# Performance work log

Hardware: AMD Instinct MI355X
Metric: run time of the kernel (lower is better)

## Reference

```python
import jax, jax.numpy as jnp
import numpy as np

B, T, D, H, E, K, OUT = 4, 1024, 512, 1024, 8, 2, 512
TEMP = 1.0      # current_temperature == max_temperature at init
LN_EPS = 1e-5   # torch LayerNorm default
MI_EPS = 1e-6


def _ln(x, g, b):
    mu = jnp.mean(x, -1, keepdims=True)
    var = jnp.mean((x - mu) ** 2, -1, keepdims=True)
    return (x - mu) * jax.lax.rsqrt(var + LN_EPS) * g + b


def setup_inputs() -> dict:
    key = jax.random.key(0)
    ks = jax.random.split(key, 16)
    s = 0.02
    return {
        "x": jax.random.normal(ks[0], (B, T, D), jnp.float32),
        # Router
        "Wmap": jax.random.normal(ks[1], (D, D * E), jnp.float32) * s,
        "bmap": jnp.zeros((D * E,), jnp.float32),
        "Wr": jax.random.normal(ks[2], (D, D), jnp.float32) * s,
        "br": jnp.zeros((D,), jnp.float32),
        # Stacked expert MLP (3 linear+GELU+LayerNorm blocks; dropout is eval no-op)
        "W1": jax.random.normal(ks[3], (E, D, H), jnp.float32) * s,
        "b1": jnp.zeros((E, H), jnp.float32),
        "g1": jnp.ones((E, H), jnp.float32),
        "beta1": jnp.zeros((E, H), jnp.float32),
        "W2": jax.random.normal(ks[4], (E, H, H), jnp.float32) * s,
        "b2": jnp.zeros((E, H), jnp.float32),
        "g2": jnp.ones((E, H), jnp.float32),
        "beta2": jnp.zeros((E, H), jnp.float32),
        "W3": jax.random.normal(ks[5], (E, H, H), jnp.float32) * s,
        "b3": jnp.zeros((E, H), jnp.float32),
        "g3": jnp.ones((E, H), jnp.float32),
        "beta3": jnp.zeros((E, H), jnp.float32),
        # out_linear: Linear(H, OUT) + GELU + LayerNorm(OUT)
        "Wo": jax.random.normal(ks[6], (H, OUT), jnp.float32) * s,
        "bo": jnp.zeros((OUT,), jnp.float32),
        "go": jnp.ones((OUT,), jnp.float32),
        "beta_o": jnp.zeros((OUT,), jnp.float32),
    }


def reference(x, Wmap, bmap, Wr, br,
              W1, b1, g1, beta1, W2, b2, g2, beta2, W3, b3, g3, beta3,
              Wo, bo, go, beta_o):
    Bx, Tx, Dx = x.shape
    Ex = W1.shape[0]
    # Router: per-token, per-expert embeddings [B,T,E,D]
    re = (x @ Wmap + bmap).reshape(Bx, Tx, Ex, Dx) @ Wr + br
    # Laplace gating (faithful to source: topk of NEGATED exp(-d/T))
    dist = jnp.linalg.norm(x[:, :, None, :] - re, axis=-1)   # [B,T,E]
    sim = jnp.exp(-dist / TEMP)
    vals, idx = jax.lax.top_k(-sim, K)                       # vals are negative
    probs = vals / jnp.sum(vals, -1, keepdims=True)          # neg/neg -> positive, sums to 1

    N = Bx * Tx
    xf = x.reshape(N, Dx)
    pf = probs.reshape(N, K)
    idf = idx.reshape(N, K)
    # Dense gate matrix [N,E]: gating weight per token per expert (0 if unselected).
    gate = jnp.zeros((N, Ex), x.dtype).at[jnp.arange(N)[:, None], idf].add(pf)

    # Stacked expert MLP on all tokens; gating zeros out unselected experts (same math
    # as the masked gather/index_add dispatch in the source).
    h = jax.nn.gelu(jnp.einsum('nd,edh->neh', xf, W1) + b1, approximate=False)
    h = _ln(h, g1, beta1)
    h = jax.nn.gelu(jnp.einsum('neh,ehf->nef', h, W2) + b2, approximate=False)
    h = _ln(h, g2, beta2)
    h = jax.nn.gelu(jnp.einsum('neh,ehf->nef', h, W3) + b3, approximate=False)
    h = _ln(h, g3, beta3)                                    # [N,E,H]
    combined = jnp.einsum('ne,neh->nh', gate, h).reshape(Bx, Tx, -1)

    out = _ln(jax.nn.gelu(combined @ Wo + bo, approximate=False), go, beta_o)

    # Stand-in for RunningMarginalMI.compute_mi_loss (source class unavailable):
    # negative mutual information between marginal and per-token slot distributions.
    pm = jnp.mean(pf, 0)
    ent_loss = jnp.sum(pm * jnp.log(pm + MI_EPS)) - jnp.mean(jnp.sum(pf * jnp.log(pf + MI_EPS), -1))
    return out, ent_loss
```

## Files before the change

### kernel.cpp

```cpp
#include <hip/hip_runtime.h>
#include <hip/hip_bf16.h>
#include <math.h>

typedef __hip_bfloat16 bf16;
typedef unsigned short u16;
typedef __attribute__((ext_vector_type(8))) short short8;
typedef __attribute__((ext_vector_type(4))) float f32x4;

#define NTOK 4096
#define DD   512
#define EE   8
#define DE   4096
#define HH   1024
#define OUTD 512
#define ATOT 8192
#define APAD 8320
#define MAXT 72
#define FCAP 1024
#define DMARGIN 1e-4
#define RSPLIT 4

struct Tile { int e, row0, rows; };

__device__ __forceinline__ float b2f(u16 u){ return __uint_as_float(((unsigned)u)<<16); }

__device__ __forceinline__ float gelu_f(float x){
  return 0.5f * x * (1.0f + erff(x * 0.7071067811865476f));
}

__device__ __forceinline__ void gl2lds(const bf16* g, bf16* l){
  __builtin_amdgcn_global_load_lds((const __attribute__((address_space(1))) void*)g,
                                   (__attribute__((address_space(3))) void*)l, 16, 0, 0);
}

__device__ __forceinline__ f32x4 mfma16(short8 a, short8 b, f32x4 c){
  return __builtin_amdgcn_mfma_f32_16x16x32_bf16(a, b, c, 0, 0, 0);
}

template<bool GATHER>
__device__ __forceinline__ void kloop(const bf16* __restrict__ A, int lda,
                                      const int* __restrict__ rowmap, int m0,
                                      const bf16* __restrict__ BT, int ldb, int n0,
                                      int K, bf16* As, bf16* Bs, f32x4 acc[4][4]){
  const int t = threadIdx.x;
  const int r = t>>2;
  const int sw = (t&3) ^ ((t>>3)&3);
  int ar0 = m0 + r, ar1 = m0 + 64 + r;
  if (GATHER){
    ar0 = rowmap[ar0 < ATOT ? ar0 : ATOT-1];
    ar1 = rowmap[ar1 < ATOT ? ar1 : ATOT-1];
  }
  const bf16* ap0 = A + (long)ar0*lda + sw*8;
  const bf16* ap1 = A + (long)ar1*lda + sw*8;
  const bf16* bp0 = BT + (long)(n0 + r)*ldb + sw*8;
  const bf16* bp1 = bp0 + (long)64*ldb;
  const int wave = t>>6, lane = t&63;
  const int qr = wave>>1, qc = wave&1, ln = lane&15, kq = lane>>4;
  const int slot = kq ^ ((ln>>1)&3);
  const bf16* ard = As + (qr*64 + ln)*32 + slot*8;
  const bf16* brd = Bs + (qc*64 + ln)*32 + slot*8;
  gl2lds(ap0, As + t*8);
  gl2lds(ap1, As + 2048 + t*8);
  gl2lds(bp0, Bs + t*8);
  gl2lds(bp1, Bs + 2048 + t*8);
  for (int k0 = 0; k0 < K; k0 += 32){
    __syncthreads();
    short8 a[4], b[4];
    #pragma unroll
    for (int i=0;i<4;i++) a[i] = *(const short8*)(ard + i*512);
    #pragma unroll
    for (int j=0;j<4;j++) b[j] = *(const short8*)(brd + j*512);
    __syncthreads();
    int k1 = k0 + 32;
    if (k1 < K){
      gl2lds(ap0 + k1, As + t*8);
      gl2lds(ap1 + k1, As + 2048 + t*8);
      gl2lds(bp0 + k1, Bs + t*8);
      gl2lds(bp1 + k1, Bs + 2048 + t*8);
    }
    #pragma unroll
    for (int i=0;i<4;i++)
      #pragma unroll
      for (int j=0;j<4;j++)
        acc[i][j] = mfma16(a[i], b[j], acc[i][j]);
  }
}

__device__ __forceinline__ void kloop2(const bf16* __restrict__ A0, const bf16* __restrict__ A1,
                                       int lda, int m0,
                                       const bf16* __restrict__ B0, const bf16* __restrict__ B1,
                                       int ldb, int n0, int K,
                                       bf16* As0, bf16* As1, bf16* Bs0, bf16* Bs1,
                                       f32x4 acc[4][4]){
  const int t = threadIdx.x;
  const int r = t>>2;
  const int sw = (t&3) ^ ((t>>3)&3);
  const long aoff0 = (long)(m0 + r)*lda + sw*8;
  const long aoff1 = (long)(m0 + 64 + r)*lda + sw*8;
  const long boff0 = (long)(n0 + r)*ldb + sw*8;
  const long boff1 = boff0 + (long)64*ldb;
  const int wave = t>>6, lane = t&63;
  const int qr = wave>>1, qc = wave&1, ln = lane&15, kq = lane>>4;
  const int slot = kq ^ ((ln>>1)&3);
  const int ao = (qr*64 + ln)*32 + slot*8;
  const int bo = (qc*64 + ln)*32 + slot*8;
  gl2lds(A0 + aoff0, As0 + t*8);
  gl2lds(A0 + aoff1, As0 + 2048 + t*8);
  gl2lds(A1 + aoff0, As1 + t*8);
  gl2lds(A1 + aoff1, As1 + 2048 + t*8);
  gl2lds(B0 + boff0, Bs0 + t*8);
  gl2lds(B0 + boff1, Bs0 + 2048 + t*8);
  gl2lds(B1 + boff0, Bs1 + t*8);
  gl2lds(B1 + boff1, Bs1 + 2048 + t*8);
  for (int k0 = 0; k0 < K; k0 += 32){
    __syncthreads();
    short8 a0[4], a1[4], b0[4], b1[4];
    #pragma unroll
    for (int i=0;i<4;i++){
      a0[i] = *(const short8*)(As0 + ao + i*512);
      a1[i] = *(const short8*)(As1 + ao + i*512);
    }
    #pragma unroll
    for (int j=0;j<4;j++){
      b0[j] = *(const short8*)(Bs0 + bo + j*512);
      b1[j] = *(const short8*)(Bs1 + bo + j*512);
    }
    __syncthreads();
    int k1 = k0 + 32;
    if (k1 < K){
      gl2lds(A0 + aoff0 + k1, As0 + t*8);
      gl2lds(A0 + aoff1 + k1, As0 + 2048 + t*8);
      gl2lds(A1 + aoff0 + k1, As1 + t*8);
      gl2lds(A1 + aoff1 + k1, As1 + 2048 + t*8);
      gl2lds(B0 + boff0 + k1, Bs0 + t*8);
      gl2lds(B0 + boff1 + k1, Bs0 + 2048 + t*8);
      gl2lds(B1 + boff0 + k1, Bs1 + t*8);
      gl2lds(B1 + boff1 + k1, Bs1 + 2048 + t*8);
    }
    #pragma unroll
    for (int i=0;i<4;i++)
      #pragma unroll
      for (int j=0;j<4;j++){
        acc[i][j] = mfma16(a0[i], b0[j], acc[i][j]);
        acc[i][j] = mfma16(a0[i], b1[j], acc[i][j]);
        acc[i][j] = mfma16(a1[i], b0[j], acc[i][j]);
      }
  }
}

__device__ __forceinline__ void kloop3(const bf16* __restrict__ A0, const bf16* __restrict__ A1,
                                       const bf16* __restrict__ A2, int lda, int m0,
                                       const bf16* __restrict__ B0, const bf16* __restrict__ B1,
                                       const bf16* __restrict__ B2, int ldb, int n0, int K,
                                       bf16* As0, bf16* As1, bf16* As2,
                                       bf16* Bs0, bf16* Bs1, bf16* Bs2,
                                       f32x4 acc[4][4]){
  const int t = threadIdx.x;
  const int r = t>>2;
  const int sw = (t&3) ^ ((t>>3)&3);
  const long aoff0 = (long)(m0 + r)*lda + sw*8;
  const long aoff1 = (long)(m0 + 64 + r)*lda + sw*8;
  const long boff0 = (long)(n0 + r)*ldb + sw*8;
  const long boff1 = boff0 + (long)64*ldb;
  const int wave = t>>6, lane = t&63;
  const int qr = wave>>1, qc = wave&1, ln = lane&15, kq = lane>>4;
  const int slot = kq ^ ((ln>>1)&3);
  const int ao = (qr*64 + ln)*32 + slot*8;
  const int bo = (qc*64 + ln)*32 + slot*8;
  gl2lds(A0 + aoff0, As0 + t*8);
  gl2lds(A0 + aoff1, As0 + 2048 + t*8);
  gl2lds(A1 + aoff0, As1 + t*8);
  gl2lds(A1 + aoff1, As1 + 2048 + t*8);
  gl2lds(A2 + aoff0, As2 + t*8);
  gl2lds(A2 + aoff1, As2 + 2048 + t*8);
  gl2lds(B0 + boff0, Bs0 + t*8);
  gl2lds(B0 + boff1, Bs0 + 2048 + t*8);
  gl2lds(B1 + boff0, Bs1 + t*8);
  gl2lds(B1 + boff1, Bs1 + 2048 + t*8);
  gl2lds(B2 + boff0, Bs2 + t*8);
  gl2lds(B2 + boff1, Bs2 + 2048 + t*8);
  for (int k0 = 0; k0 < K; k0 += 32){
    __syncthreads();
    short8 a0[4], a1[4], a2[4], b0[4], b1[4], b2[4];
    #pragma unroll
    for (int i=0;i<4;i++){
      a0[i] = *(const short8*)(As0 + ao + i*512);
      a1[i] = *(const short8*)(As1 + ao + i*512);
      a2[i] = *(const short8*)(As2 + ao + i*512);
    }
    #pragma unroll
    for (int j=0;j<4;j++){
      b0[j] = *(const short8*)(Bs0 + bo + j*512);
      b1[j] = *(const short8*)(Bs1 + bo + j*512);
      b2[j] = *(const short8*)(Bs2 + bo + j*512);
    }
    __syncthreads();
    int k1 = k0 + 32;
    if (k1 < K){
      gl2lds(A0 + aoff0 + k1, As0 + t*8);
      gl2lds(A0 + aoff1 + k1, As0 + 2048 + t*8);
      gl2lds(A1 + aoff0 + k1, As1 + t*8);
      gl2lds(A1 + aoff1 + k1, As1 + 2048 + t*8);
      gl2lds(A2 + aoff0 + k1, As2 + t*8);
      gl2lds(A2 + aoff1 + k1, As2 + 2048 + t*8);
      gl2lds(B0 + boff0 + k1, Bs0 + t*8);
      gl2lds(B0 + boff1 + k1, Bs0 + 2048 + t*8);
      gl2lds(B1 + boff0 + k1, Bs1 + t*8);
      gl2lds(B1 + boff1 + k1, Bs1 + 2048 + t*8);
      gl2lds(B2 + boff0 + k1, Bs2 + t*8);
      gl2lds(B2 + boff1 + k1, Bs2 + 2048 + t*8);
    }
    #pragma unroll
    for (int i=0;i<4;i++)
      #pragma unroll
      for (int j=0;j<4;j++){
        acc[i][j] = mfma16(a0[i], b0[j], acc[i][j]);
        acc[i][j] = mfma16(a0[i], b1[j], acc[i][j]);
        acc[i][j] = mfma16(a1[i], b0[j], acc[i][j]);
        acc[i][j] = mfma16(a0[i], b2[j], acc[i][j]);
        acc[i][j] = mfma16(a1[i], b1[j], acc[i][j]);
        acc[i][j] = mfma16(a2[i], b0[j], acc[i][j]);
      }
  }
}

#define EPI_SETUP \
  const int t = threadIdx.x, wave=t>>6, lane=t&63; \
  const int qr=wave>>1, qc=wave&1, ln=lane&15, kq=lane>>4; (void)qr;

#define ACC_INIT \
  f32x4 acc[4][4]; \
  _Pragma("unroll") for (int i=0;i<4;i++) _Pragma("unroll") for (int j=0;j<4;j++) \
    acc[i][j] = (f32x4){0.f,0.f,0.f,0.f};

__device__ __forceinline__ void split3_body(const float* __restrict__ in,
    bf16* __restrict__ oh, bf16* __restrict__ om, bf16* __restrict__ ol, int b, int n4){
  int i = b*256 + threadIdx.x;
  if (i >= n4) return;
  float4 v = ((const float4*)in)[i];
  float vv[4] = {v.x, v.y, v.z, v.w};
  u16 hs[4], ms[4], ls[4];
  #pragma unroll
  for (int c=0;c<4;c++){
    bf16 h = __float2bfloat16(vv[c]); float r1 = vv[c] - __bfloat162float(h);
    bf16 m = __float2bfloat16(r1);    float r2 = r1 - __bfloat162float(m);
    bf16 l = __float2bfloat16(r2);
    hs[c]=*(u16*)&h; ms[c]=*(u16*)&m; ls[c]=*(u16*)&l;
  }
  ((ushort4*)oh)[i] = (ushort4){hs[0],hs[1],hs[2],hs[3]};
  ((ushort4*)om)[i] = (ushort4){ms[0],ms[1],ms[2],ms[3]};
  ((ushort4*)ol)[i] = (ushort4){ls[0],ls[1],ls[2],ls[3]};
}

__device__ __forceinline__ void tsplit3_body(const float* __restrict__ in,
    bf16* __restrict__ oh, bf16* __restrict__ om, bf16* __restrict__ ol,
    int R, int C, int bx, int by, float* tile ){
  int r0 = by*64, c0 = bx*64;
  int t = threadIdx.x, lr = t>>4, lc = (t&15)*4;
  #pragma unroll
  for (int it=0; it<4; it++){
    int rr = it*16 + lr;
    float4 v = *(const float4*)(in + (long)(r0+rr)*C + c0 + lc);
    tile[rr*65+lc]=v.x; tile[rr*65+lc+1]=v.y; tile[rr*65+lc+2]=v.z; tile[rr*65+lc+3]=v.w;
  }
  __syncthreads();
  #pragma unroll
  for (int it=0; it<4; it++){
    int cc = it*16 + lr;
    u16 hs[4], ms[4], ls[4];
    #pragma unroll
    for (int j=0;j<4;j++){
      float v = tile[(lc+j)*65+cc];
      bf16 h = __float2bfloat16(v); float r1 = v - __bfloat162float(h);
      bf16 m = __float2bfloat16(r1); float r2 = r1 - __bfloat162float(m);
      bf16 l = __float2bfloat16(r2);
      hs[j]=*(u16*)&h; ms[j]=*(u16*)&m; ls[j]=*(u16*)&l;
    }
    long oi = (long)(c0+cc)*R + r0 + lc;
    *(ushort4*)((u16*)oh + oi) = (ushort4){hs[0],hs[1],hs[2],hs[3]};
    *(ushort4*)((u16*)om + oi) = (ushort4){ms[0],ms[1],ms[2],ms[3]};
    *(ushort4*)((u16*)ol + oi) = (ushort4){ls[0],ls[1],ls[2],ls[3]};
  }
}

__device__ __forceinline__ void cvtT_body(const float* __restrict__ in,
    bf16* __restrict__ out, int R, int C, int bx, int by, int bz, float* tile){
  long zb = (long)bz * R * C;
  int r0 = by*64, c0 = bx*64;
  int t = threadIdx.x, lr = t>>4, lc = (t&15)*4;
  #pragma unroll
  for (int it=0; it<4; it++){
    int rr = it*16 + lr;
    float4 v = *(const float4*)(in + zb + (long)(r0+rr)*C + c0 + lc);
    tile[rr*65+lc]=v.x; tile[rr*65+lc+1]=v.y; tile[rr*65+lc+2]=v.z; tile[rr*65+lc+3]=v.w;
  }
  __syncthreads();
  #pragma unroll
  for (int it=0; it<4; it++){
    int cc = it*16 + lr;
    u16 hs[4];
    #pragma unroll
    for (int j=0;j<4;j++){
      bf16 h = __float2bfloat16(tile[(lc+j)*65+cc]);
      hs[j]=*(u16*)&h;
    }
    *(ushort4*)((u16*)out + zb + (long)(c0+cc)*R + r0 + lc) = (ushort4){hs[0],hs[1],hs[2],hs[3]};
  }
}

__device__ __forceinline__ void cvec_body(const float* __restrict__ bmap,
    const float* __restrict__ Wr, const float* __restrict__ br, float* __restrict__ cvec, int b){
  int id = b*256 + threadIdx.x;
  int e = id >> 9, j = id & 511;
  float s = 0.f;
  for (int k=0;k<512;k++) s += bmap[e*512+k] * Wr[k*512 + j];
  cvec[id] = s + br[j];
}

__global__ __launch_bounds__(256) void k_prep(const float* __restrict__ x,
    const float* __restrict__ Wmap, const float* __restrict__ Wr,
    const float* __restrict__ bmap, const float* __restrict__ br,
    const float* __restrict__ W1, const float* __restrict__ W2,
    const float* __restrict__ W3, const float* __restrict__ Wo,
    bf16* xh, bf16* xm, bf16* xl,
    bf16* Wm_h, bf16* Wm_m, bf16* Wm_l,
    bf16* WrT_h, bf16* WrT_m, bf16* WrT_l, float* cvec,
    bf16* W1T, bf16* W2T, bf16* W3T, bf16* WoT){
  __shared__ float tile[64*65];
  int b = blockIdx.x;
  if (b < 2048){ split3_body(x, xh, xm, xl, b, 524288); return; }
  b -= 2048;
  if (b < 2048){ split3_body(Wmap, Wm_h, Wm_m, Wm_l, b, 524288); return; }
  b -= 2048;
  if (b < 64){ tsplit3_body(Wr, WrT_h, WrT_m, WrT_l, 512, 512, b&7, b>>3, tile); return; }
  b -= 64;
  if (b < 16){ cvec_body(bmap, Wr, br, cvec, b); return; }
  b -= 16;
  if (b < 1024){ cvtT_body(W1, W1T, 512, 1024, b&15, (b>>4)&7, b>>7, tile); return; }
  b -= 1024;
  if (b < 2048){ cvtT_body(W2, W2T, 1024, 1024, b&15, (b>>4)&15, b>>8, tile); return; }
  b -= 2048;
  if (b < 2048){ cvtT_body(W3, W3T, 1024, 1024, b&15, (b>>4)&15, b>>8, tile); return; }
  b -= 2048;
  cvtT_body(Wo, WoT, 1024, 512, b&7, b>>3, 0, tile);
}
#define PREP_BLOCKS 9424

__global__ __launch_bounds__(256) void k_gemm_MT(
    const bf16* __restrict__ Rh, const bf16* __restrict__ Rm, const bf16* __restrict__ Rl,
    const bf16* __restrict__ Wh, const bf16* __restrict__ Wm, const bf16* __restrict__ Wl,
    bf16* __restrict__ MTh, bf16* __restrict__ MTm, float* __restrict__ M32){
  __shared__ __align__(16) bf16 As0[4096], As1[4096], As2[4096],
                                Bs0[4096], Bs1[4096], Bs2[4096];
  int m0 = blockIdx.x*128, n0 = blockIdx.y*128, e = blockIdx.z;
  ACC_INIT
  kloop3(Rh, Rm, Rl, 512, m0, Wh + e*512, Wm + e*512, Wl + e*512, DE, n0, 512,
         As0, As1, As2, Bs0, Bs1, Bs2, acc);
  EPI_SETUP
  int cg[4];
  #pragma unroll
  for (int j=0;j<4;j++) cg[j] = n0 + qc*64 + j*16 + ln;
  long eb = (long)e*512*512;
  #pragma unroll
  for (int i=0;i<4;i++)
    #pragma unroll
    for (int r=0;r<4;r++){
      long base = eb + (long)(m0 + qr*64 + i*16 + kq*4 + r) * 512;
      #pragma unroll
      for (int j=0;j<4;j++){
        float v = acc[i][j][r];
        bf16 h = __float2bfloat16(v); float r1 = v - __bfloat162float(h);
        bf16 m = __float2bfloat16(r1);
        MTh[base + cg[j]] = h; MTm[base + cg[j]] = m; M32[base + cg[j]] = v;
      }
    }
}

__global__ __launch_bounds__(256) void k_gemm_re(
    const bf16* __restrict__ xh, const bf16* __restrict__ xm,
    const bf16* __restrict__ MTh, const bf16* __restrict__ MTm,
    const float* __restrict__ cvec, const float* __restrict__ x, double* __restrict__ dist2){
  __shared__ __align__(16) bf16 As0[4096], As1[4096], Bs0[4096], Bs1[4096];
  int m0 = blockIdx.x*128, n0 = blockIdx.y*128, e = blockIdx.z;
  ACC_INIT
  long eb = (long)e*512*512;
  kloop2(xh, xm, 512, m0, MTh + eb, MTm + eb, 512, n0, 512,
         As0, As1, Bs0, Bs1, acc);
  EPI_SETUP
  int cg[4]; float cv[4];
  #pragma unroll
  for (int j=0;j<4;j++){ cg[j] = n0 + qc*64 + j*16 + ln; cv[j] = cvec[e*512 + cg[j]]; }
  #pragma unroll
  for (int i=0;i<4;i++)
    #pragma unroll
    for (int r=0;r<4;r++){
      int rg = m0 + qr*64 + i*16 + kq*4 + r;
      const float* xr = x + (long)rg*512;
      double s = 0.0;
      #pragma unroll
      for (int j=0;j<4;j++){
        float re = acc[i][j][r] + cv[j];
        float d  = xr[cg[j]] - re;
        s += (double)d * (double)d;
      }
      s += __shfl_xor(s,1); s += __shfl_xor(s,2); s += __shfl_xor(s,4); s += __shfl_xor(s,8);
      if (ln == 0) atomicAdd(&dist2[(long)rg*EE + e], s);
    }
}

__global__ __launch_bounds__(256) void k_gemm_exp(const Tile* __restrict__ table,
    const bf16* __restrict__ A, int lda, const int* __restrict__ rowmap,
    const bf16* __restrict__ Wt, long wstride, int ldb, int K,
    const float* __restrict__ bias, int ncols, bf16* __restrict__ out, int ldo){
  Tile tc = table[blockIdx.x];
  if (tc.e < 0) return;
  __shared__ __align__(16) bf16 As[4096], Bs[4096];
  int n0 = blockIdx.y*128;
  ACC_INIT
  const bf16* BT = Wt + (long)tc.e*wstride;
  if (rowmap) kloop<true >(A, lda, rowmap, tc.row0, BT, ldb, n0, K, As, Bs, acc);
  else        kloop<false>(A, lda, nullptr, tc.row0, BT, ldb, n0, K, As, Bs, acc);
  EPI_SETUP
  const float* bp = bias + (long)tc.e*ncols;
  int cg[4]; float bv[4];
  #pragma unroll
  for (int j=0;j<4;j++){ cg[j] = n0 + qc*64 + j*16 + ln; bv[j] = bp[cg[j]]; }
  #pragma unroll
  for (int i=0;i<4;i++)
    #pragma unroll
    for (int r=0;r<4;r++){
      int rl = qr*64 + i*16 + kq*4 + r;
      if (rl < tc.rows){
        bf16* op = out + (long)(tc.row0 + rl)*ldo;
        #pragma unroll
        for (int j=0;j<4;j++)
          op[cg[j]] = __float2bfloat16(gelu_f(acc[i][j][r] + bv[j]));
      }
    }
}

__global__ __launch_bounds__(256) void k_gemm_go(const bf16* __restrict__ A,
    const bf16* __restrict__ WoT, const float* __restrict__ bias, bf16* __restrict__ out){
  __shared__ __align__(16) bf16 As[4096], Bs[4096];
  int m0 = blockIdx.x*128, n0 = blockIdx.y*128;
  ACC_INIT
  kloop<false>(A, HH, nullptr, m0, WoT, HH, n0, HH, As, Bs, acc);
  EPI_SETUP
  int cg[4]; float bv[4];
  #pragma unroll
  for (int j=0;j<4;j++){ cg[j] = n0 + qc*64 + j*16 + ln; bv[j] = bias[cg[j]]; }
  #pragma unroll
  for (int i=0;i<4;i++)
    #pragma unroll
    for (int r=0;r<4;r++){
      long base = (long)(m0 + qr*64 + i*16 + kq*4 + r) * OUTD;
      #pragma unroll
      for (int j=0;j<4;j++)
        out[base + cg[j]] = __float2bfloat16(gelu_f(acc[i][j][r] + bv[j]));
    }
}

__global__ __launch_bounds__(256) void k_select(const double* __restrict__ dist2,
    float* __restrict__ selp, int* __restrict__ seli, int* __restrict__ counts,
    float* __restrict__ entacc, int* __restrict__ flaglist, int* __restrict__ nflag){
  __shared__ int hc[EE];
  int t = threadIdx.x;
  if (t < EE) hc[t] = 0;
  __syncthreads();
  int n = blockIdx.x*256 + t;
  double d0 = -1.0, d1 = -1.0, d2 = -1.0; int i0 = 0, i1 = 0;
  #pragma unroll
  for (int e=0;e<EE;e++){
    double d = sqrt(dist2[(long)n*EE + e]);
    if (d > d0){ d2 = d1; d1 = d0; i1 = i0; d0 = d; i0 = e; }
    else if (d > d1){ d2 = d1; d1 = d; i1 = e; }
    else if (d > d2){ d2 = d; }
  }
  if (d1 - d2 < DMARGIN){ int p = atomicAdd(nflag, 1); flaglist[p & (FCAP-1)] = n; }
  double s0 = exp(-d0), s1 = exp(-d1);
  double den = s0 + s1;
  float p0 = (float)(s0/den), p1 = (float)(s1/den);
  selp[2*n] = p0; selp[2*n+1] = p1;
  seli[2*n] = i0; seli[2*n+1] = i1;
  atomicAdd(&hc[i0], 1); atomicAdd(&hc[i1], 1);
  float a0 = p0, a1 = p1;
  float a2 = p0*logf(p0+1e-6f) + p1*logf(p1+1e-6f);
  #pragma unroll
  for (int m=32;m;m>>=1){ a0 += __shfl_down(a0,m); a1 += __shfl_down(a1,m); a2 += __shfl_down(a2,m); }
  if ((t&63)==0){ atomicAdd(&entacc[0], a0); atomicAdd(&entacc[1], a1); atomicAdd(&entacc[2], a2); }
  __syncthreads();
  if (t < EE) atomicAdd(&counts[t], hc[t]);
}

__global__ __launch_bounds__(256) void k_rescue(const int* __restrict__ flaglist,
    const int* __restrict__ nflag, const float* __restrict__ x,
    const float* __restrict__ M32, const float* __restrict__ cvec,
    double* __restrict__ rbuf4){
  __shared__ float xs[512];
  __shared__ double wsum[4];
  int t = threadIdx.x, w = t>>6, l = t&63;
  int nf = *nflag; if (nf > FCAP) nf = FCAP;
  int work = nf * EE * RSPLIT;
  for (int wid = blockIdx.x; wid < work; wid += gridDim.x){
    int pid = wid >> 2, chunk = wid & (RSPLIT-1);
    int f = pid >> 3, e = pid & 7;
    int n = flaglist[f];
    xs[t] = x[(long)n*512 + t]; xs[t+256] = x[(long)n*512 + 256 + t];
    __syncthreads();
    const float* Me = M32 + ((long)e << 18);
    const float* xp = xs + l*8;
    float x0=xp[0], x1=xp[1], x2=xp[2], x3=xp[3], x4=xp[4], x5=xp[5], x6=xp[6], x7=xp[7];
    double s = 0.0;
    int j0 = chunk*128 + w*32;
    for (int rb = 0; rb < 32; rb += 8){
      double d[8];
      #pragma unroll
      for (int rr=0; rr<8; rr++){
        const float* Mr = Me + (long)(j0 + rb + rr)*512 + l*8;
        float4 a = *(const float4*)Mr, b = *(const float4*)(Mr+4);
        d[rr] = (double)a.x*x0 + (double)a.y*x1 + (double)a.z*x2 + (double)a.w*x3
              + (double)b.x*x4 + (double)b.y*x5 + (double)b.z*x6 + (double)b.w*x7;
      }
      #pragma unroll
      for (int m=32;m;m>>=1){
        #pragma unroll
        for (int rr=0; rr<8; rr++) d[rr] += __shfl_down(d[rr], m);
      }
      if (l == 0){
        #pragma unroll
        for (int rr=0; rr<8; rr++){
          int j = j0 + rb + rr;
          double diff = (double)xs[j] - (d[rr] + (double)cvec[e*512 + j]);
          s += diff*diff;
        }
      }
    }
    if (l == 0) wsum[w] = s;
    __syncthreads();
    if (t == 0) rbuf4[wid] = wsum[0]+wsum[1]+wsum[2]+wsum[3];
    __syncthreads();
  }
}

__global__ __launch_bounds__(256) void k_scan(const int* __restrict__ flaglist,
    const int* __restrict__ nflag, const double* __restrict__ rbuf4,
    float* __restrict__ selp, int* __restrict__ seli,
    int* __restrict__ counts, float* __restrict__ entacc,
    int* __restrict__ cursors, Tile* __restrict__ table, float* __restrict__ entout){
  int t = threadIdx.x;
  int nf = *nflag; if (nf > FCAP) nf = FCAP;
  for (int idx = t; idx < nf; idx += 256){
    int n = flaglist[idx];
    double d0=-1.0, d1=-1.0; int i0=0, i1=0;
    #pragma unroll
    for (int e=0;e<EE;e++){
      const double* rp = rbuf4 + ((long)(idx*EE + e))*RSPLIT;
      double d = sqrt(rp[0] + rp[1] + rp[2] + rp[3]);
      if (d > d0){ d1=d0; i1=i0; d0=d; i0=e; }
      else if (d > d1){ d1=d; i1=e; }
    }
    double s0 = exp(-d0), s1 = exp(-d1), den = s0+s1;
    float p0 = (float)(s0/den), p1 = (float)(s1/den);
    int o0 = seli[2*n], o1 = seli[2*n+1];
    float q0 = selp[2*n], q1 = selp[2*n+1];
    if (o0 != i0 || o1 != i1){
      atomicSub(&counts[o0], 1); atomicSub(&counts[o1], 1);
      atomicAdd(&counts[i0], 1); atomicAdd(&counts[i1], 1);
      seli[2*n] = i0; seli[2*n+1] = i1;
    }
    atomicAdd(&entacc[0], p0 - q0);
    atomicAdd(&entacc[1], p1 - q1);
    atomicAdd(&entacc[2], (p0*logf(p0+1e-6f) + p1*logf(p1+1e-6f))
                        - (q0*logf(q0+1e-6f) + q1*logf(q1+1e-6f)));
    selp[2*n] = p0; selp[2*n+1] = p1;
  }
  __threadfence();
  __syncthreads();
  if (t != 0) return;
  int off = 0, ti = 0;
  for (int e=0;e<EE;e++){
    cursors[e] = off;
    int c = counts[e];
    for (int r=0;r<c;r+=128){
      table[ti].e = e; table[ti].row0 = off + r;
      table[ti].rows = (c - r < 128) ? (c - r) : 128; ti++;
    }
    off += c;
  }
  for (; ti<MAXT; ti++){ table[ti].e = -1; table[ti].row0 = 0; table[ti].rows = 0; }
  float pm0 = entacc[0] * (1.0f/NTOK), pm1 = entacc[1] * (1.0f/NTOK);
  *entout = pm0*logf(pm0 + 1e-6f) + pm1*logf(pm1 + 1e-6f) - entacc[2] * (1.0f/NTOK);
}

__global__ __launch_bounds__(256) void k_place(const int* __restrict__ seli,
    const float* __restrict__ selp, int* __restrict__ cursors,
    int* __restrict__ atok, float* __restrict__ ap, int* __restrict__ aslot,
    int* __restrict__ aexp){
  int id = blockIdx.x*256 + threadIdx.x;
  int e = seli[id];
  int pos = atomicAdd(&cursors[e], 1);
  atok[pos] = id >> 1;
  ap[pos]   = selp[id];
  aslot[pos]= id & 1;
  aexp[pos] = e;
}

__device__ __forceinline__ void blkred2(float& s, float& q, int t){
  #pragma unroll
  for (int m=32;m;m>>=1){ s += __shfl_down(s,m); q += __shfl_down(q,m); }
  __shared__ float shs[4], shq[4];
  if ((t&63)==0){ shs[t>>6] = s; shq[t>>6] = q; }
  __syncthreads();
  s = shs[0]+shs[1]+shs[2]+shs[3];
  q = shq[0]+shq[1]+shq[2]+shq[3];
}

__global__ __launch_bounds__(256) void k_ln_mid(const bf16* __restrict__ in, bf16* __restrict__ out,
    const float* __restrict__ g, const float* __restrict__ be, const int* __restrict__ aexp){
  int row = blockIdx.x, t = threadIdx.x;
  const ushort4 u = *(const ushort4*)((const u16*)in + (long)row*HH + t*4);
  float v0=b2f(u.x), v1=b2f(u.y), v2=b2f(u.z), v3=b2f(u.w);
  float s = v0+v1+v2+v3;
  float q = v0*v0+v1*v1+v2*v2+v3*v3;
  blkred2(s, q, t);
  float mu = s*(1.0f/HH);
  float rs = rsqrtf(q*(1.0f/HH) - mu*mu + 1e-5f);
  int e = aexp[row];
  const float4 ug = *(const float4*)(g  + (long)e*HH + t*4);
  const float4 ub = *(const float4*)(be + (long)e*HH + t*4);
  bf16* op = out + (long)row*HH + t*4;
  op[0] = __float2bfloat16((v0-mu)*rs*ug.x + ub.x);
  op[1] = __float2bfloat16((v1-mu)*rs*ug.y + ub.y);
  op[2] = __float2bfloat16((v2-mu)*rs*ug.z + ub.z);
  op[3] = __float2bfloat16((v3-mu)*rs*ug.w + ub.w);
}

__global__ __launch_bounds__(256) void k_ln3(const bf16* __restrict__ in, float* __restrict__ slots,
    const float* __restrict__ g, const float* __restrict__ be, const int* __restrict__ aexp,
    const int* __restrict__ atok, const int* __restrict__ aslot, const float* __restrict__ ap){
  int row = blockIdx.x, t = threadIdx.x;
  const ushort4 u = *(const ushort4*)((const u16*)in + (long)row*HH + t*4);
  float v0=b2f(u.x), v1=b2f(u.y), v2=b2f(u.z), v3=b2f(u.w);
  float s = v0+v1+v2+v3;
  float q = v0*v0+v1*v1+v2*v2+v3*v3;
  blkred2(s, q, t);
  float mu = s*(1.0f/HH);
  float rs = rsqrtf(q*(1.0f/HH) - mu*mu + 1e-5f);
  int e = aexp[row];
  const float4 ug = *(const float4*)(g  + (long)e*HH + t*4);
  const float4 ub = *(const float4*)(be + (long)e*HH + t*4);
  float p = ap[row];
  float* op = slots + ((long)atok[row]*2 + aslot[row])*HH + t*4;
  op[0] = p*((v0-mu)*rs*ug.x + ub.x);
  op[1] = p*((v1-mu)*rs*ug.y + ub.y);
  op[2] = p*((v2-mu)*rs*ug.z + ub.z);
  op[3] = p*((v3-mu)*rs*ug.w + ub.w);
}

__global__ __launch_bounds__(256) void k_comb(const float* __restrict__ slots, bf16* __restrict__ comb){
  long i = (long)blockIdx.x*256 + threadIdx.x;
  long n = i >> 10, c = i & 1023;
  comb[i] = __float2bfloat16(slots[n*2*HH + c] + slots[(n*2+1)*HH + c]);
}

__global__ __launch_bounds__(256) void k_lnout(const bf16* __restrict__ in, float* __restrict__ dout,
    const float* __restrict__ g, const float* __restrict__ be, const float* __restrict__ entout){
  int row = blockIdx.x, t = threadIdx.x;
  const bf16* ip = in + (long)row*OUTD + t*2;
  float v0 = __bfloat162float(ip[0]), v1 = __bfloat162float(ip[1]);
  float s = v0+v1, q = v0*v0+v1*v1;
  blkred2(s, q, t);
  float mu = s*(1.0f/OUTD);
  float rs = rsqrtf(q*(1.0f/OUTD) - mu*mu + 1e-5f);
  float g0 = g[t*2], g1v = g[t*2+1];
  float b0 = be[t*2], b1v = be[t*2+1];
  float* op = dout + (long)row*OUTD + t*2;
  op[0] = (v0-mu)*rs*g0 + b0;
  op[1] = (v1-mu)*rs*g1v + b1v;
  if (row==0 && t==0) dout[(long)NTOK*OUTD] = *entout;
}

extern "C" void kernel_launch(void* const* d_in, const int* in_sizes, int n_in,
                              void* d_out, int out_size, void* d_ws, size_t ws_size,
                              hipStream_t stream){
  (void)in_sizes; (void)n_in; (void)out_size; (void)ws_size;
  const float* x    = (const float*)d_in[0];
  const float* Wmap = (const float*)d_in[1];
  const float* bmap = (const float*)d_in[2];
  const float* Wr   = (const float*)d_in[3];
  const float* br   = (const float*)d_in[4];
  const float* W1   = (const float*)d_in[5];
  const float* b1   = (const float*)d_in[6];
  const float* g1   = (const float*)d_in[7];
  const float* be1  = (const float*)d_in[8];
  const float* W2   = (const float*)d_in[9];
  const float* b2   = (const float*)d_in[10];
  const float* g2   = (const float*)d_in[11];
  const float* be2  = (const float*)d_in[12];
  const float* W3   = (const float*)d_in[13];
  const float* b3   = (const float*)d_in[14];
  const float* g3   = (const float*)d_in[15];
  const float* be3  = (const float*)d_in[16];
  const float* Wo   = (const float*)d_in[17];
  const float* bo   = (const float*)d_in[18];
  const float* go   = (const float*)d_in[19];
  const float* beo  = (const float*)d_in[20];

  char* ws = (char*)d_ws;
  size_t o = 0;
  auto take = [&](size_t b){ size_t r = o; o += (b + 255) & ~(size_t)255; return r; };
  size_t o_xh   = take((size_t)NTOK*DD*2);
  size_t o_xm   = take((size_t)NTOK*DD*2);
  size_t o_xl   = take((size_t)NTOK*DD*2);
  size_t o_R1   = take((size_t)APAD*HH*2);
  size_t o_R2   = take((size_t)APAD*HH*2);
  size_t o_W1T  = take((size_t)EE*HH*DD*2);
  size_t o_W2T  = take((size_t)EE*HH*HH*2);
  size_t o_W3T  = take((size_t)EE*HH*HH*2);
  size_t o_WoT  = take((size_t)OUTD*HH*2);
  size_t o_dist2= take((size_t)NTOK*EE*8);
  size_t o_cnt  = take(64);
  size_t o_ent  = take(64);
  size_t o_nfl  = take(64);
  size_t o_cur  = take(64);
  size_t o_eout = take(64);
  size_t o_flag = take((size_t)FCAP*4);
  size_t o_rbuf = take((size_t)FCAP*EE*RSPLIT*8);
  size_t o_selp = take((size_t)NTOK*2*4);
  size_t o_seli = take((size_t)NTOK*2*4);
  size_t o_atok = take((size_t)ATOT*4);
  size_t o_ap   = take((size_t)ATOT*4);
  size_t o_aslt = take((size_t)ATOT*4);
  size_t o_aexp = take((size_t)ATOT*4);
  size_t o_tab  = take((size_t)MAXT*sizeof(Tile));

  bf16* xh=(bf16*)(ws+o_xh); bf16* xm=(bf16*)(ws+o_xm); bf16* xl=(bf16*)(ws+o_xl);
  bf16* Wm_h=(bf16*)(ws+o_R1);
  bf16* Wm_m=(bf16*)(ws+o_R1+ 4194304);
  bf16* Wm_l=(bf16*)(ws+o_R1+ 8388608);
  bf16* WrT_h=(bf16*)(ws+o_R1+12582912);
  bf16* WrT_m=(bf16*)(ws+o_R1+13107200);
  bf16* WrT_l=(bf16*)(ws+o_R1+13631488);
  float* cvec=(float*)(ws+o_R1+14155776);
  bf16* MT_h=(bf16*)(ws+o_R2);
  bf16* MT_m=(bf16*)(ws+o_R2+4194304);
  float* M32=(float*)(ws+o_R2+8388608);
  bf16* hba=(bf16*)(ws+o_R1);
  bf16* hbb=(bf16*)(ws+o_R2);
  bf16* W1T=(bf16*)(ws+o_W1T); bf16* W2T=(bf16*)(ws+o_W2T); bf16* W3T=(bf16*)(ws+o_W3T);
  bf16* WoT=(bf16*)(ws+o_WoT);
  float* slots=(float*)(ws+o_W2T);
  bf16* comb=(bf16*)(ws+o_xm);
  bf16* obuf=(bf16*)(ws+o_W1T);
  double* dist2=(double*)(ws+o_dist2);
  int* counts=(int*)(ws+o_cnt); float* entacc=(float*)(ws+o_ent);
  int* nflag=(int*)(ws+o_nfl);
  int* cursors=(int*)(ws+o_cur); float* entout=(float*)(ws+o_eout);
  int* flaglist=(int*)(ws+o_flag);
  double* rbuf4=(double*)(ws+o_rbuf);
  float* selp=(float*)(ws+o_selp); int* seli=(int*)(ws+o_seli);
  int* atok=(int*)(ws+o_atok); float* ap=(float*)(ws+o_ap);
  int* aslot=(int*)(ws+o_aslt); int* aexp=(int*)(ws+o_aexp);
  Tile* table=(Tile*)(ws+o_tab);

  hipMemsetAsync(ws + o_dist2, 0, (o_nfl + 64) - o_dist2, stream);

  k_prep<<<PREP_BLOCKS,256,0,stream>>>(x, Wmap, Wr, bmap, br, W1, W2, W3, Wo,
      xh, xm, xl, Wm_h, Wm_m, Wm_l, WrT_h, WrT_m, WrT_l, cvec, W1T, W2T, W3T, WoT);

  k_gemm_MT<<<dim3(4,4,8),256,0,stream>>>(WrT_h, WrT_m, WrT_l, Wm_h, Wm_m, Wm_l,
                                          MT_h, MT_m, M32);
  k_gemm_re<<<dim3(32,4,8),256,0,stream>>>(xh, xm, MT_h, MT_m, cvec, x, dist2);
  k_select<<<16,256,0,stream>>>(dist2, selp, seli, counts, entacc, flaglist, nflag);
  k_rescue<<<2048,256,0,stream>>>(flaglist, nflag, x, M32, cvec, rbuf4);
  k_scan<<<1,256,0,stream>>>(flaglist, nflag, rbuf4, selp, seli, counts, entacc,
                             cursors, table, entout);
  k_place<<<32,256,0,stream>>>(seli, selp, cursors, atok, ap, aslot, aexp);

  k_gemm_exp<<<dim3(MAXT,8),256,0,stream>>>(table, xh, DD, atok,
      W1T, (long)HH*DD, DD, DD, b1, HH, hba, HH);
  k_ln_mid<<<ATOT,256,0,stream>>>(hba, hbb, g1, be1, aexp);
  k_gemm_exp<<<dim3(MAXT,8),256,0,stream>>>(table, hbb, HH, nullptr,
      W2T, (long)HH*HH, HH, HH, b2, HH, hba, HH);
  k_ln_mid<<<ATOT,256,0,stream>>>(hba, hbb, g2, be2, aexp);
  k_gemm_exp<<<dim3(MAXT,8),256,0,stream>>>(table, hbb, HH, nullptr,
      W3T, (long)HH*HH, HH, HH, b3, HH, hba, HH);
  k_ln3<<<ATOT,256,0,stream>>>(hba, slots, g3, be3, aexp, atok, aslot, ap);
  k_comb<<<16384,256,0,stream>>>(slots, comb);
  k_gemm_go<<<dim3(32,4),256,0,stream>>>(comb, WoT, bo, obuf);
  k_lnout<<<NTOK,256,0,stream>>>(obuf, (float*)d_out, go, beo, entout);
}
```

Baseline: 546.3 us.

## Load A fragments directly from global memory and double-buffer B tiles in LDS

In kloop and kloop2, A-operand fragments are now read straight from global memory into registers in MFMA layout instead of being staged through LDS. B tiles get double buffering, which drops the second barrier per k-step. This reduces LDS traffic and synchronisation. In exchange, A reads become uncoalesced 16-byte per-lane loads that wait on global latency inside the k-loop, and the 2x2 waves in a block each re-read overlapping A rows from cache.

```diff
diff --git a/kernel.cpp b/kernel.cpp
--- a/kernel.cpp
+++ b/kernel.cpp
@@ -41,48 +41,44 @@
 __device__ __forceinline__ void kloop(const bf16* __restrict__ A, int lda,
                                       const int* __restrict__ rowmap, int m0,
                                       const bf16* __restrict__ BT, int ldb, int n0,
-                                      int K, bf16* As, bf16* Bs, f32x4 acc[4][4]){
+                                      int K, bf16 (*Bs)[4096], f32x4 acc[4][4]){
   const int t = threadIdx.x;
   const int r = t>>2;
   const int sw = (t&3) ^ ((t>>3)&3);
-  int ar0 = m0 + r, ar1 = m0 + 64 + r;
-  if (GATHER){
-    ar0 = rowmap[ar0 < ATOT ? ar0 : ATOT-1];
-    ar1 = rowmap[ar1 < ATOT ? ar1 : ATOT-1];
-  }
-  const bf16* ap0 = A + (long)ar0*lda + sw*8;
-  const bf16* ap1 = A + (long)ar1*lda + sw*8;
   const bf16* bp0 = BT + (long)(n0 + r)*ldb + sw*8;
   const bf16* bp1 = bp0 + (long)64*ldb;
   const int wave = t>>6, lane = t&63;
   const int qr = wave>>1, qc = wave&1, ln = lane&15, kq = lane>>4;
   const int slot = kq ^ ((ln>>1)&3);
-  const bf16* ard = As + (qr*64 + ln)*32 + slot*8;
-  const bf16* brd = Bs + (qc*64 + ln)*32 + slot*8;
-  gl2lds(ap0, As + t*8);
-  gl2lds(ap1, As + 2048 + t*8);
-  gl2lds(bp0, Bs + t*8);
-  gl2lds(bp1, Bs + 2048 + t*8);
+  const int bo = (qc*64 + ln)*32 + slot*8;
+  const bf16* arp[4];
+  #pragma unroll
+  for (int i=0;i<4;i++){
+    int row = m0 + qr*64 + i*16 + ln;
+    if (GATHER) row = rowmap[row < ATOT ? row : ATOT-1];
+    arp[i] = A + (long)row*lda + kq*8;
+  }
+  gl2lds(bp0, Bs[0] + t*8);
+  gl2lds(bp1, Bs[0] + 2048 + t*8);
+  int cur = 0;
   for (int k0 = 0; k0 < K; k0 += 32){
     __syncthreads();
     short8 a[4], b[4];
     #pragma unroll
-    for (int i=0;i<4;i++) a[i] = *(const short8*)(ard + i*512);
-    #pragma unroll
-    for (int j=0;j<4;j++) b[j] = *(const short8*)(brd + j*512);
-    __syncthreads();
+    for (int i=0;i<4;i++) a[i] = *(const short8*)(arp[i] + k0);
+    #pragma unroll
+    for (int j=0;j<4;j++) b[j] = *(const short8*)(Bs[cur] + bo + j*512);
     int k1 = k0 + 32;
     if (k1 < K){
-      gl2lds(ap0 + k1, As + t*8);
-      gl2lds(ap1 + k1, As + 2048 + t*8);
-      gl2lds(bp0 + k1, Bs + t*8);
-      gl2lds(bp1 + k1, Bs + 2048 + t*8);
+      gl2lds(bp0 + k1, Bs[cur^1] + t*8);
+      gl2lds(bp1 + k1, Bs[cur^1] + 2048 + t*8);
     }
     #pragma unroll
     for (int i=0;i<4;i++)
       #pragma unroll
       for (int j=0;j<4;j++)
         acc[i][j] = mfma16(a[i], b[j], acc[i][j]);
+    cur ^= 1;
   }
 }
 
@@ -90,52 +86,49 @@
                                        int lda, int m0,
                                        const bf16* __restrict__ B0, const bf16* __restrict__ B1,
                                        int ldb, int n0, int K,
-                                       bf16* As0, bf16* As1, bf16* Bs0, bf16* Bs1,
+                                       bf16 (*Bs0)[4096], bf16 (*Bs1)[4096],
                                        f32x4 acc[4][4]){
   const int t = threadIdx.x;
   const int r = t>>2;
   const int sw = (t&3) ^ ((t>>3)&3);
-  const long aoff0 = (long)(m0 + r)*lda + sw*8;
-  const long aoff1 = (long)(m0 + 64 + r)*lda + sw*8;
   const long boff0 = (long)(n0 + r)*ldb + sw*8;
   const long boff1 = boff0 + (long)64*ldb;
   const int wave = t>>6, lane = t&63;
   const int qr = wave>>1, qc = wave&1, ln = lane&15, kq = lane>>4;
   const int slot = kq ^ ((ln>>1)&3);
-  const int ao = (qr*64 + ln)*32 + slot*8;
   const int bo = (qc*64 + ln)*32 + slot*8;
-  gl2lds(A0 + aoff0, As0 + t*8);
-  gl2lds(A0 + aoff1, As0 + 2048 + t*8);
-  gl2lds(A1 + aoff0, As1 + t*8);
-  gl2lds(A1 + aoff1, As1 + 2048 + t*8);
-  gl2lds(B0 + boff0, Bs0 + t*8);
-  gl2lds(B0 + boff1, Bs0 + 2048 + t*8);
-  gl2lds(B1 + boff0, Bs1 + t*8);
-  gl2lds(B1 + boff1, Bs1 + 2048 + t*8);
+  const bf16* arp0[4];
+  const bf16* arp1[4];
+  #pragma unroll
+  for (int i=0;i<4;i++){
+    int row = m0 + qr*64 + i*16 + ln;
+    arp0[i] = A0 + (long)row*lda + kq*8;
+    arp1[i] = A1 + (long)row*lda + kq*8;
+  }
+  gl2lds(B0 + boff0, Bs0[0] + t*8);
+  gl2lds(B0 + boff1, Bs0[0] + 2048 + t*8);
+  gl2lds(B1 + boff0, Bs1[0] + t*8);
+  gl2lds(B1 + boff1, Bs1[0] + 2048 + t*8);
+  int cur = 0;
   for (int k0 = 0; k0 < K; k0 += 32){
     __syncthreads();
     short8 a0[4], a1[4], b0[4], b1[4];
     #pragma unroll
     for (int i=0;i<4;i++){
-      a0[i] = *(const short8*)(As0 + ao + i*512);
-      a1[i] = *(const short8*)(As1 + ao + i*512);
+      a0[i] = *(const short8*)(arp0[i] + k0);
+      a1[i] = *(const short8*)(arp1[i] + k0);
     }
     #pragma unroll
     for (int j=0;j<4;j++){
-      b0[j] = *(const short8*)(Bs0 + bo + j*512);
-      b1[j] = *(const short8*)(Bs1 + bo + j*512);
-    }
-    __syncthreads();
+      b0[j] = *(const short8*)(Bs0[cur] + bo + j*512);
+      b1[j] = *(const short8*)(Bs1[cur] + bo + j*512);
+    }
     int k1 = k0 + 32;
     if (k1 < K){
-      gl2lds(A0 + aoff0 + k1, As0 + t*8);
-      gl2lds(A0 + aoff1 + k1, As0 + 2048 + t*8);
-      gl2lds(A1 + aoff0 + k1, As1 + t*8);
-      gl2lds(A1 + aoff1 + k1, As1 + 2048 + t*8);
-      gl2lds(B0 + boff0 + k1, Bs0 + t*8);
-      gl2lds(B0 + boff1 + k1, Bs0 + 2048 + t*8);
-      gl2lds(B1 + boff0 + k1, Bs1 + t*8);
-      gl2lds(B1 + boff1 + k1, Bs1 + 2048 + t*8);
+      gl2lds(B0 + boff0 + k1, Bs0[cur^1] + t*8);
+      gl2lds(B0 + boff1 + k1, Bs0[cur^1] + 2048 + t*8);
+      gl2lds(B1 + boff0 + k1, Bs1[cur^1] + t*8);
+      gl2lds(B1 + boff1 + k1, Bs1[cur^1] + 2048 + t*8);
     }
     #pragma unroll
     for (int i=0;i<4;i++)
@@ -145,6 +138,7 @@
         acc[i][j] = mfma16(a0[i], b1[j], acc[i][j]);
         acc[i][j] = mfma16(a1[i], b0[j], acc[i][j]);
       }
+    cur ^= 1;
   }
 }
 
@@ -380,12 +374,12 @@
     const bf16* __restrict__ xh, const bf16* __restrict__ xm,
     const bf16* __restrict__ MTh, const bf16* __restrict__ MTm,
     const float* __restrict__ cvec, const float* __restrict__ x, double* __restrict__ dist2){
-  __shared__ __align__(16) bf16 As0[4096], As1[4096], Bs0[4096], Bs1[4096];
+  __shared__ __align__(16) bf16 Bs0[2][4096], Bs1[2][4096];
   int m0 = blockIdx.x*128, n0 = blockIdx.y*128, e = blockIdx.z;
   ACC_INIT
   long eb = (long)e*512*512;
   kloop2(xh, xm, 512, m0, MTh + eb, MTm + eb, 512, n0, 512,
-         As0, As1, Bs0, Bs1, acc);
+         Bs0, Bs1, acc);
   EPI_SETUP
   int cg[4]; float cv[4];
   #pragma unroll
@@ -414,12 +408,12 @@
     const float* __restrict__ bias, int ncols, bf16* __restrict__ out, int ldo){
   Tile tc = table[blockIdx.x];
   if (tc.e < 0) return;
-  __shared__ __align__(16) bf16 As[4096], Bs[4096];
+  __shared__ __align__(16) bf16 Bs[2][4096];
   int n0 = blockIdx.y*128;
   ACC_INIT
   const bf16* BT = Wt + (long)tc.e*wstride;
-  if (rowmap) kloop<true >(A, lda, rowmap, tc.row0, BT, ldb, n0, K, As, Bs, acc);
-  else        kloop<false>(A, lda, nullptr, tc.row0, BT, ldb, n0, K, As, Bs, acc);
+  if (rowmap) kloop<true >(A, lda, rowmap, tc.row0, BT, ldb, n0, K, Bs, acc);
+  else        kloop<false>(A, lda, nullptr, tc.row0, BT, ldb, n0, K, Bs, acc);
   EPI_SETUP
   const float* bp = bias + (long)tc.e*ncols;
   int cg[4]; float bv[4];
@@ -441,10 +435,10 @@
 
 __global__ __launch_bounds__(256) void k_gemm_go(const bf16* __restrict__ A,
     const bf16* __restrict__ WoT, const float* __restrict__ bias, bf16* __restrict__ out){
-  __shared__ __align__(16) bf16 As[4096], Bs[4096];
+  __shared__ __align__(16) bf16 Bs[2][4096];
   int m0 = blockIdx.x*128, n0 = blockIdx.y*128;
   ACC_INIT
-  kloop<false>(A, HH, nullptr, m0, WoT, HH, n0, HH, As, Bs, acc);
+  kloop<false>(A, HH, nullptr, m0, WoT, HH, n0, HH, Bs, acc);
   EPI_SETUP
   int cg[4]; float bv[4];
   #pragma unroll
```

Result: slower. 650.7 us (+19.1%).
